# Optimization experiments

Measured on AMD Instinct MI355X. Metric: run time of the kernel, lower is better.

Reference implementation:

```python
import jax, jax.numpy as jnp
import numpy as np

IN_DIM = 768
OUT_DIM = 768
NUM = IN_DIM * OUT_DIM
NUM_F = 8


def setup_inputs() -> dict:
    key = jax.random.key(0)
    k1, k2, k3 = jax.random.split(key, 3)
    x = jax.random.normal(k1, (32, 12, 64), dtype=jnp.float32)
    grid = jnp.arange(NUM_F, dtype=jnp.float32) + 1.0  # torch: arange(num_f)+1
    coef = jax.random.uniform(k2, (NUM, NUM_F), dtype=jnp.float32)
    bias_w = jax.random.normal(k3, (1, OUT_DIM), dtype=jnp.float32)
    scale_base = jnp.ones((NUM,), dtype=jnp.float32)
    scale_sp = jnp.ones((NUM,), dtype=jnp.float32)
    return {"x": x, "grid": grid, "coef": coef, "bias_w": bias_w,
            "scale_base": scale_base, "scale_sp": scale_sp}


def reference(x, grid, coef, bias_w, scale_base, scale_sp):
    batch = x.shape[0]
    out_dim = bias_w.shape[1]
    num = coef.shape[0]
    in_dim = num // out_dim
    # flatten [B, C, F] -> [B, in_dim]
    x2 = x.reshape(batch, in_dim)
    # broadcast each input feature to every output: [B, out_dim, in_dim] -> [num, B]
    xr = jnp.broadcast_to(x2[:, None, :], (batch, out_dim, in_dim)).reshape(batch, num).T
    base = jax.nn.silu(xr)                                  # [num, B]
    # sin basis: [num, num_f, B]
    f = jnp.sin(grid[None, :, None] * xr[:, None, :])
    f_out = jnp.einsum('ij,ijk->ik', coef, f)               # [num, B]
    f_out = (scale_sp[:, None] * f_out + scale_base[:, None] * base).T  # [B, num]
    y = f_out.reshape(batch, out_dim, in_dim).sum(axis=2)   # [B, out_dim]
    return y + bias_w
```

## Files before the change

kernel.cpp:

```cpp
#include <hip/hip_runtime.h>
#include <math.h>

#define IN_DIM 768
#define OUT_DIM 768
#define BATCH 32
#define NUM_F 8
#define SPAD 12

#define O_TILE 16
#define I_SPLIT 16
#define I_CHUNK (IN_DIM / I_SPLIT)

__global__ __launch_bounds__(256) void build_S(const float* __restrict__ x,
                                               const float* __restrict__ grid,
                                               const float* __restrict__ bias_w,
                                               float* __restrict__ S,
                                               float* __restrict__ y) {
    int idx = blockIdx.x * 256 + threadIdx.x;
    if (idx >= BATCH * IN_DIM) return;
    float xv = x[idx];
    float* out = S + (size_t)idx * SPAD;
    float4 a, b4;
    a.x  = __sinf(grid[0] * xv);
    a.y  = __sinf(grid[1] * xv);
    a.z  = __sinf(grid[2] * xv);
    a.w  = __sinf(grid[3] * xv);
    b4.x = __sinf(grid[4] * xv);
    b4.y = __sinf(grid[5] * xv);
    b4.z = __sinf(grid[6] * xv);
    b4.w = __sinf(grid[7] * xv);
    *(float4*)(out)     = a;
    *(float4*)(out + 4) = b4;
    out[8] = xv / (1.0f + __expf(-xv));
    y[idx] = bias_w[idx % OUT_DIM];
}

__global__ __launch_bounds__(256) void fused_reduce(const float* __restrict__ S,
                                                    const float* __restrict__ coef,
                                                    const float* __restrict__ scale_base,
                                                    const float* __restrict__ scale_sp,
                                                    float* __restrict__ y) {
    __shared__ float red[8 * 512];
    const int t  = threadIdx.x;
    const int b  = t & 31;
    const int g  = t >> 5;
    const int ob = blockIdx.x / I_SPLIT;
    const int is = blockIdx.x % I_SPLIT;
    const int o0 = ob * O_TILE;
    const int i0 = is * I_CHUNK;

    float acc[O_TILE];
#pragma unroll
    for (int ol = 0; ol < O_TILE; ++ol) acc[ol] = 0.0f;

    for (int i = i0 + g; i < i0 + I_CHUNK; i += 8) {
        const float4* sp = (const float4*)(S + (size_t)(b * IN_DIM + i) * SPAD);
        const float4 sA = sp[0];
        const float4 sB = sp[1];
        const float  s8 = S[(size_t)(b * IN_DIM + i) * SPAD + 8];
#pragma unroll
        for (int ol = 0; ol < O_TILE; ++ol) {
            const int n = (o0 + ol) * IN_DIM + i;
            const float4* cp = (const float4*)(coef + (size_t)n * 8);
            const float4 c0 = cp[0];
            const float4 c1 = cp[1];
            const float ssp = scale_sp[n];
            const float sb  = scale_base[n];
            float dot = c0.x * sA.x + c0.y * sA.y + c0.z * sA.z + c0.w * sA.w
                      + c1.x * sB.x + c1.y * sB.y + c1.z * sB.z + c1.w * sB.w;
            acc[ol] += ssp * dot + sb * s8;
        }
    }

#pragma unroll
    for (int ol = 0; ol < O_TILE; ++ol)
        red[g * 512 + b * O_TILE + ol] = acc[ol];
    __syncthreads();

#pragma unroll
    for (int rep = 0; rep < 2; ++rep) {
        const int idx2 = t + rep * 256;
        const int b2  = idx2 >> 4;
        const int ol2 = idx2 & 15;
        float sum = 0.0f;
#pragma unroll
        for (int g2 = 0; g2 < 8; ++g2) sum += red[g2 * 512 + idx2];
        atomicAdd(&y[b2 * OUT_DIM + o0 + ol2], sum);
    }
}

extern "C" void kernel_launch(void* const* d_in, const int* in_sizes, int n_in,
                              void* d_out, int out_size, void* d_ws, size_t ws_size,
                              hipStream_t stream) {
    const float* x          = (const float*)d_in[0];
    const float* grid       = (const float*)d_in[1];
    const float* coef       = (const float*)d_in[2];
    const float* bias_w     = (const float*)d_in[3];
    const float* scale_base = (const float*)d_in[4];
    const float* scale_sp   = (const float*)d_in[5];
    float* y = (float*)d_out;
    float* S = (float*)d_ws;

    build_S<<<(BATCH * IN_DIM + 255) / 256, 256, 0, stream>>>(x, grid, bias_w, S, y);
    fused_reduce<<<(OUT_DIM / O_TILE) * I_SPLIT, 256, 0, stream>>>(S, coef, scale_base,
                                                                   scale_sp, y);
}
```

Measured before the change: 106.2 us.

## Fuse sin/silu basis computation into reduction kernel via shared memory

Removes the separate build_S pass that wrote the sine/silu basis to global workspace. Each block now computes the basis for its 32-column input chunk directly into shared memory and reads it from there in the reduction loop. The input split changes from 16 to 24 chunks, so there are more blocks and more atomics. The trade-off is redundant sin computation: each input chunk is recomputed by all 48 output tiles.

```diff
diff --git a/kernel.cpp b/kernel.cpp
--- a/kernel.cpp
+++ b/kernel.cpp
@@ -1,90 +1,95 @@
 #include <hip/hip_runtime.h>
 #include <math.h>
 
-#define IN_DIM 768
+#define IN_DIM  768
 #define OUT_DIM 768
-#define BATCH 32
-#define NUM_F 8
-#define SPAD 12
+#define BATCH   32
+#define NUM_F   8
 
-#define O_TILE 16
-#define I_SPLIT 16
-#define I_CHUNK (IN_DIM / I_SPLIT)
+#define O_TILE  16
+#define I_CHUNK 32
+#define I_SPLIT (IN_DIM / I_CHUNK)
 
-__global__ __launch_bounds__(256) void build_S(const float* __restrict__ x,
-                                               const float* __restrict__ grid,
-                                               const float* __restrict__ bias_w,
-                                               float* __restrict__ S,
-                                               float* __restrict__ y) {
-    int idx = blockIdx.x * 256 + threadIdx.x;
-    if (idx >= BATCH * IN_DIM) return;
-    float xv = x[idx];
-    float* out = S + (size_t)idx * SPAD;
-    float4 a, b4;
-    a.x  = __sinf(grid[0] * xv);
-    a.y  = __sinf(grid[1] * xv);
-    a.z  = __sinf(grid[2] * xv);
-    a.w  = __sinf(grid[3] * xv);
-    b4.x = __sinf(grid[4] * xv);
-    b4.y = __sinf(grid[5] * xv);
-    b4.z = __sinf(grid[6] * xv);
-    b4.w = __sinf(grid[7] * xv);
-    *(float4*)(out)     = a;
-    *(float4*)(out + 4) = b4;
-    out[8] = xv / (1.0f + __expf(-xv));
-    y[idx] = bias_w[idx % OUT_DIM];
+#define SROW   (I_CHUNK + 1)
+#define SPLANE (BATCH * SROW)
+#define SMEM_FLOATS (9 * SPLANE)
+
+__global__ __launch_bounds__(768) void init_y(const float* __restrict__ bias_w,
+                                              float* __restrict__ y) {
+    y[blockIdx.x * OUT_DIM + threadIdx.x] = bias_w[threadIdx.x];
 }
 
-__global__ __launch_bounds__(256) void fused_reduce(const float* __restrict__ S,
-                                                    const float* __restrict__ coef,
-                                                    const float* __restrict__ scale_base,
-                                                    const float* __restrict__ scale_sp,
-                                                    float* __restrict__ y) {
-    __shared__ float red[8 * 512];
+__global__ __launch_bounds__(256) void fused(const float* __restrict__ x,
+                                             const float* __restrict__ grid,
+                                             const float* __restrict__ coef,
+                                             const float* __restrict__ scale_base,
+                                             const float* __restrict__ scale_sp,
+                                             float* __restrict__ y) {
+    __shared__ float smem[SMEM_FLOATS];
+
     const int t  = threadIdx.x;
-    const int b  = t & 31;
-    const int g  = t >> 5;
-    const int ob = blockIdx.x / I_SPLIT;
-    const int is = blockIdx.x % I_SPLIT;
+    const int is = blockIdx.x;
+    const int ob = blockIdx.y;
+    const int i0 = is * I_CHUNK;
     const int o0 = ob * O_TILE;
-    const int i0 = is * I_CHUNK;
 
+    float gv[NUM_F];
+#pragma unroll
+    for (int j = 0; j < NUM_F; ++j) gv[j] = grid[j];
+
+#pragma unroll
+    for (int p = t; p < BATCH * I_CHUNK; p += 256) {
+        const int il = p & (I_CHUNK - 1);
+        const int b  = p >> 5;
+        const float xv = x[b * IN_DIM + i0 + il];
+#pragma unroll
+        for (int j = 0; j < NUM_F; ++j)
+            smem[j * SPLANE + b * SROW + il] = __sinf(gv[j] * xv);
+        smem[8 * SPLANE + b * SROW + il] = xv / (1.0f + __expf(-xv));
+    }
+    __syncthreads();
+
+    const int b = t & 31;
+    const int g = t >> 5;
     float acc[O_TILE];
 #pragma unroll
     for (int ol = 0; ol < O_TILE; ++ol) acc[ol] = 0.0f;
 
-    for (int i = i0 + g; i < i0 + I_CHUNK; i += 8) {
-        const float4* sp = (const float4*)(S + (size_t)(b * IN_DIM + i) * SPAD);
-        const float4 sA = sp[0];
-        const float4 sB = sp[1];
-        const float  s8 = S[(size_t)(b * IN_DIM + i) * SPAD + 8];
+#pragma unroll
+    for (int k = 0; k < I_CHUNK / 8; ++k) {
+        const int il = g + k * 8;
+        const int i  = i0 + il;
+        float s[9];
+#pragma unroll
+        for (int j = 0; j < 9; ++j) s[j] = smem[j * SPLANE + b * SROW + il];
 #pragma unroll
         for (int ol = 0; ol < O_TILE; ++ol) {
-            const int n = (o0 + ol) * IN_DIM + i;
-            const float4* cp = (const float4*)(coef + (size_t)n * 8);
-            const float4 c0 = cp[0];
-            const float4 c1 = cp[1];
+            const size_t n = (size_t)(o0 + ol) * IN_DIM + i;
+            const float4 c0 = *(const float4*)(coef + n * 8);
+            const float4 c1 = *(const float4*)(coef + n * 8 + 4);
             const float ssp = scale_sp[n];
             const float sb  = scale_base[n];
-            float dot = c0.x * sA.x + c0.y * sA.y + c0.z * sA.z + c0.w * sA.w
-                      + c1.x * sB.x + c1.y * sB.y + c1.z * sB.z + c1.w * sB.w;
-            acc[ol] += ssp * dot + sb * s8;
+            const float dot = c0.x * s[0] + c0.y * s[1] + c0.z * s[2] + c0.w * s[3]
+                            + c1.x * s[4] + c1.y * s[5] + c1.z * s[6] + c1.w * s[7];
+            acc[ol] += ssp * dot + sb * s[8];
         }
     }
 
+    __syncthreads();
+
 #pragma unroll
     for (int ol = 0; ol < O_TILE; ++ol)
-        red[g * 512 + b * O_TILE + ol] = acc[ol];
+        smem[(g * O_TILE + ol) * 32 + b] = acc[ol];
     __syncthreads();
 
 #pragma unroll
     for (int rep = 0; rep < 2; ++rep) {
         const int idx2 = t + rep * 256;
-        const int b2  = idx2 >> 4;
-        const int ol2 = idx2 & 15;
+        const int b2  = idx2 & 31;
+        const int ol2 = idx2 >> 5;
         float sum = 0.0f;
 #pragma unroll
-        for (int g2 = 0; g2 < 8; ++g2) sum += red[g2 * 512 + idx2];
+        for (int g2 = 0; g2 < 8; ++g2) sum += smem[(g2 * O_TILE + ol2) * 32 + b2];
         atomicAdd(&y[b2 * OUT_DIM + o0 + ol2], sum);
     }
 }
@@ -99,9 +104,9 @@
     const float* scale_base = (const float*)d_in[4];
     const float* scale_sp   = (const float*)d_in[5];
     float* y = (float*)d_out;
-    float* S = (float*)d_ws;
+    (void)d_ws; (void)ws_size;
 
-    build_S<<<(BATCH * IN_DIM + 255) / 256, 256, 0, stream>>>(x, grid, bias_w, S, y);
-    fused_reduce<<<(OUT_DIM / O_TILE) * I_SPLIT, 256, 0, stream>>>(S, coef, scale_base,
-                                                                   scale_sp, y);
+    init_y<<<BATCH, OUT_DIM, 0, stream>>>(bias_w, y);
+    dim3 grid2(I_SPLIT, OUT_DIM / O_TILE);
+    fused<<<grid2, 256, 0, stream>>>(x, grid, coef, scale_base, scale_sp, y);
 }
```

Result: slower. 139.8 us (+31.7%).
